# Performance work log

Measured on AMD Instinct MI355X. Metric: run time of the kernel, lower is better.

The kernel has to match this reference:

```python
import jax, jax.numpy as jnp
import numpy as np

N = 100000   # nodes per node type
E = 400000   # edges per relation
IN = 128     # input feature dim
HID = 128    # hidden_channels
H = 8        # heads
D = HID // H # head dim = 16
NEG_SLOPE = 0.2
BN_EPS = 1e-5


def setup_inputs() -> dict:
    key = jax.random.key(0)
    ks = jax.random.split(key, 24)
    f32 = jnp.float32
    def rn(k, shape, s):
        return jax.random.normal(k, shape, dtype=f32) * s
    inp = {
        'x_a': jax.random.normal(ks[0], (N, IN), dtype=f32),
        'x_b': jax.random.normal(ks[1], (N, IN), dtype=f32),
        'ei_ab': jax.random.randint(ks[2], (2, E), 0, N, dtype=jnp.int32),
        'ei_ba': jax.random.randint(ks[3], (2, E), 0, N, dtype=jnp.int32),
        'ei_aa': jax.random.randint(ks[4], (2, E), 0, N, dtype=jnp.int32),
        'ei_bb': jax.random.randint(ks[5], (2, E), 0, N, dtype=jnp.int32),
        # per-node-type projections (PyG Linear, with bias)
        'W_a': rn(ks[6], (IN, HID), 0.08), 'b_a': jnp.zeros((HID,), f32),
        'W_b': rn(ks[7], (IN, HID), 0.08), 'b_b': jnp.zeros((HID,), f32),
        # per-relation node-level attention vectors [H, D]
        'att_ab_s': rn(ks[8], (H, D), 0.2), 'att_ab_d': rn(ks[9], (H, D), 0.2),
        'att_ba_s': rn(ks[10], (H, D), 0.2), 'att_ba_d': rn(ks[11], (H, D), 0.2),
        'att_aa_s': rn(ks[12], (H, D), 0.2), 'att_aa_d': rn(ks[13], (H, D), 0.2),
        'att_bb_s': rn(ks[14], (H, D), 0.2), 'att_bb_d': rn(ks[15], (H, D), 0.2),
        # semantic-level attention: k_lin (Linear HID->HID) and query q
        'Wk': rn(ks[16], (HID, HID), 0.08), 'bk': jnp.zeros((HID,), f32),
        'q': rn(ks[17], (HID,), 0.2),
        # shared BatchNorm1d affine params
        'gamma': jnp.ones((HID,), f32), 'beta': jnp.zeros((HID,), f32),
    }
    return inp


def _edge_attn(h_src, h_dst, ei, att_s, att_d, n_dst):
    # GAT-style node-level attention for one relation (PyG HANConv message path)
    src, dst = ei[0], ei[1]
    a = (h_src * att_s).sum(-1)[src] + (h_dst * att_d).sum(-1)[dst]  # [E, H]
    a = jax.nn.leaky_relu(a, NEG_SLOPE)
    amax = jax.ops.segment_max(a, dst, num_segments=n_dst)            # [n_dst, H]
    amax = jnp.where(jnp.isfinite(amax), amax, 0.0)
    ex = jnp.exp(a - amax[dst])
    denom = jax.ops.segment_sum(ex, dst, num_segments=n_dst)[dst] + 1e-16
    w = ex / denom                                                    # segment softmax
    out = jax.ops.segment_sum(w[:, :, None] * h_src[src], dst, num_segments=n_dst)
    return jax.nn.relu(out.reshape(n_dst, H * D))                     # [n_dst, HID]


def _semantic(outs, Wk, bk, q):
    # semantic-level attention over relations targeting the same dst type
    st = jnp.stack(outs)                                   # [K, N, HID]
    score = (jnp.tanh(st @ Wk + bk).mean(axis=1) * q).sum(-1)  # [K]
    attn = jax.nn.softmax(score)
    return jnp.einsum('k,knf->nf', attn, st)


def _bn(x, gamma, beta):
    # BatchNorm1d in training mode: batch stats, biased variance
    mu = x.mean(axis=0)
    var = ((x - mu) ** 2).mean(axis=0)
    return (x - mu) * jax.lax.rsqrt(var + BN_EPS) * gamma + beta


def reference(x_a, x_b, ei_ab, ei_ba, ei_aa, ei_bb, W_a, b_a, W_b, b_b,
              att_ab_s, att_ab_d, att_ba_s, att_ba_d, att_aa_s, att_aa_d,
              att_bb_s, att_bb_d, Wk, bk, q, gamma, beta):
    h_a = (x_a @ W_a + b_a).reshape(N, H, D)
    h_b = (x_b @ W_b + b_b).reshape(N, H, D)
    o_ab = _edge_attn(h_a, h_b, ei_ab, att_ab_s, att_ab_d, N)  # dst b
    o_bb = _edge_attn(h_b, h_b, ei_bb, att_bb_s, att_bb_d, N)  # dst b
    o_ba = _edge_attn(h_b, h_a, ei_ba, att_ba_s, att_ba_d, N)  # dst a
    o_aa = _edge_attn(h_a, h_a, ei_aa, att_aa_s, att_aa_d, N)  # dst a
    out_a = _semantic([o_ba, o_aa], Wk, bk, q)
    out_b = _semantic([o_ab, o_bb], Wk, bk, q)
    return _bn(out_a, gamma, beta), _bn(out_b, gamma, beta)
```

## Files before the change

### kernel.cpp

```cpp
#include <hip/hip_runtime.h>

using u16 = unsigned short;
using u32 = unsigned int;
using bf16x8 = __attribute__((ext_vector_type(8))) short;
using f32x4  = __attribute__((ext_vector_type(4))) float;

__device__ __forceinline__ float bf2f(u16 v) { return __uint_as_float(((u32)v) << 16); }
__device__ __forceinline__ float blo(u32 u) { return __uint_as_float(u << 16); }
__device__ __forceinline__ float bhi(u32 u) { return __uint_as_float(u & 0xffff0000u); }
__device__ __forceinline__ u16 f2bf(float f) {
  u32 u = __float_as_uint(f);
  u += 0x7fffu + ((u >> 16) & 1u);
  return (u16)(u >> 16);
}
__device__ __forceinline__ float fast_tanh(float x) {
  float cx = fminf(fmaxf(x, -9.f), 9.f);
  float e = __expf(2.f * cx);
  return (e - 1.f) / (e + 1.f);
}

__global__ __launch_bounds__(256) void fused1_kernel(
    const float* __restrict__ x_a, const float* __restrict__ x_b,
    const float* __restrict__ W_a, const float* __restrict__ W_b,
    const float* __restrict__ b_a, const float* __restrict__ b_b,
    const float* __restrict__ at0a, const float* __restrict__ at1a,
    const float* __restrict__ at2a, const float* __restrict__ at3a,
    const float* __restrict__ at0b, const float* __restrict__ at1b,
    const float* __restrict__ at2b, const float* __restrict__ at3b,
    u16* __restrict__ ha, u16* __restrict__ hb,
    float* __restrict__ a0a, float* __restrict__ a1a,
    float* __restrict__ a2a, float* __restrict__ a3a,
    float* __restrict__ a0b, float* __restrict__ a1b,
    float* __restrict__ a2b, float* __restrict__ a3b,
    const int* __restrict__ e0, const int* __restrict__ e1,
    const int* __restrict__ e2, const int* __restrict__ e3,
    const float* __restrict__ Wk, u16* __restrict__ WkT,
    int* __restrict__ cnt,
    int N, int E, int gproj, int gE, int interleave)
{
  __shared__ __align__(16) u16 WTl[128 * 136];
  const int tid = threadIdx.x;
  const int bid = blockIdx.x;
  const int nP = 2 * gproj, nH = 4 * gE;

  int role, idx;
  if (bid >= nP + nH) { role = 2; idx = bid - nP - nH; }
  else if (interleave) {
    int slot = bid % 3, grp = bid / 3;
    if (slot == 0) { role = 0; idx = grp; }
    else           { role = 1; idx = grp * 2 + slot - 1; }
  } else {
    if (bid < nP) { role = 0; idx = bid; }
    else          { role = 1; idx = bid - nP; }
  }

  if (role == 1) {
    const int r = idx & 3, ex = idx >> 2;
    const int* ei = (r == 0) ? e0 : (r == 1) ? e1 : (r == 2) ? e2 : e3;
    int e = ex * 256 + tid;
    if (e < E) atomicAdd(&cnt[r * N + ei[E + e]], 1);
    return;
  }
  if (role == 2) {
    int i2 = idx * 256 + tid;
    int k = i2 >> 7, n = i2 & 127;
    WkT[n * 128 + k] = f2bf(Wk[i2]);
    return;
  }

  const int ty = idx >= gproj;
  const int bx = idx - (ty ? gproj : 0);
  const float* x    = ty ? x_b : x_a;
  const float* W    = ty ? W_b : W_a;
  const float* bias = ty ? b_b : b_a;
  const float* att0 = ty ? at0b : at0a;
  const float* att1 = ty ? at1b : at1a;
  const float* att2 = ty ? at2b : at2a;
  const float* att3 = ty ? at3b : at3a;
  u16* h_out = ty ? hb : ha;
  float* al0 = ty ? a0b : a0a;
  float* al1 = ty ? a1b : a1a;
  float* al2 = ty ? a2b : a2a;
  float* al3 = ty ? a3b : a3a;

  const float4* Wg = (const float4*)W;
#pragma unroll
  for (int i = 0; i < 16; ++i) {
    int id = tid + 256 * i;
    int k = id >> 5, n4 = (id & 31) << 2;
    float4 v = Wg[id];
    WTl[(n4 + 0) * 136 + k] = f2bf(v.x);
    WTl[(n4 + 1) * 136 + k] = f2bf(v.y);
    WTl[(n4 + 2) * 136 + k] = f2bf(v.z);
    WTl[(n4 + 3) * 136 + k] = f2bf(v.w);
  }
  __syncthreads();

  const int lane = tid & 63, wl = tid >> 6;
  const int col = lane & 15, g = lane >> 4;
  const int nb = bx * 64 + wl * 16;
  const int node = nb + col;
  const bool ok = node < N;

  const int arow = min(node, N - 1);
  const float* xr = x + (size_t)arow * 128;
  bf16x8 xh[4], xlo[4];
#pragma unroll
  for (int t = 0; t < 4; ++t) {
    float4 u = *(const float4*)&xr[t * 32 + g * 8];
    float4 v = *(const float4*)&xr[t * 32 + g * 8 + 4];
    float e[8] = {u.x, u.y, u.z, u.w, v.x, v.y, v.z, v.w};
    bf16x8 h8, l8;
#pragma unroll
    for (int j = 0; j < 8; ++j) {
      u16 hbt = f2bf(e[j]);
      h8[j] = (short)hbt;
      l8[j] = (short)f2bf(e[j] - bf2f(hbt));
    }
    xh[t] = h8; xlo[t] = l8;
  }

  f32x4 acc[8];
#pragma unroll
  for (int c = 0; c < 8; ++c) {
    float4 bv = *(const float4*)&bias[c * 16 + g * 4];
    acc[c] = (f32x4){bv.x, bv.y, bv.z, bv.w};
  }

#pragma unroll
  for (int c = 0; c < 8; ++c) {
    const u16* wrow = &WTl[(c * 16 + col) * 136];
#pragma unroll
    for (int t = 0; t < 4; ++t) {
      bf16x8 wf = *(const bf16x8*)&wrow[t * 32 + g * 8];
      acc[c] = __builtin_amdgcn_mfma_f32_16x16x32_bf16(wf, xh[t],  acc[c], 0, 0, 0);
      acc[c] = __builtin_amdgcn_mfma_f32_16x16x32_bf16(wf, xlo[t], acc[c], 0, 0, 0);
    }
  }

  if (ok) {
#pragma unroll
    for (int c = 0; c < 8; ++c) {
      uint2 hv;
      hv.x = (u32)f2bf(acc[c][0]) | ((u32)f2bf(acc[c][1]) << 16);
      hv.y = (u32)f2bf(acc[c][2]) | ((u32)f2bf(acc[c][3]) << 16);
      *(uint2*)(h_out + (size_t)node * 128 + c * 16 + g * 4) = hv;
    }
  }

#pragma unroll
  for (int c = 0; c < 8; ++c) {
    float4 a0v = *(const float4*)&att0[c * 16 + g * 4];
    float4 a1v = *(const float4*)&att1[c * 16 + g * 4];
    float4 a2v = *(const float4*)&att2[c * 16 + g * 4];
    float4 a3v = *(const float4*)&att3[c * 16 + g * 4];
    float p0 = acc[c][0] * a0v.x + acc[c][1] * a0v.y + acc[c][2] * a0v.z + acc[c][3] * a0v.w;
    float p1 = acc[c][0] * a1v.x + acc[c][1] * a1v.y + acc[c][2] * a1v.z + acc[c][3] * a1v.w;
    float p2 = acc[c][0] * a2v.x + acc[c][1] * a2v.y + acc[c][2] * a2v.z + acc[c][3] * a2v.w;
    float p3 = acc[c][0] * a3v.x + acc[c][1] * a3v.y + acc[c][2] * a3v.z + acc[c][3] * a3v.w;
    p0 += __shfl_xor(p0, 16); p0 += __shfl_xor(p0, 32);
    p1 += __shfl_xor(p1, 16); p1 += __shfl_xor(p1, 32);
    p2 += __shfl_xor(p2, 16); p2 += __shfl_xor(p2, 32);
    p3 += __shfl_xor(p3, 16); p3 += __shfl_xor(p3, 32);
    if (ok && g == 0) {
      al0[node * 8 + c] = p0;
      al1[node * 8 + c] = p1;
      al2[node * 8 + c] = p2;
      al3[node * 8 + c] = p3;
    }
  }
}

__global__ __launch_bounds__(256) void scan1_kernel(int* __restrict__ data, int M,
                                                    int* __restrict__ bsum)
{
  __shared__ int ls[256];
  const int tid = threadIdx.x;
  const int base = blockIdx.x * 2048 + tid * 8;
  int v[8]; int s = 0;
#pragma unroll
  for (int j = 0; j < 8; ++j) v[j] = (base + j < M) ? data[base + j] : 0;
#pragma unroll
  for (int j = 0; j < 8; ++j) { int t = v[j]; v[j] = s; s += t; }
  ls[tid] = s;
  __syncthreads();
  for (int off = 1; off < 256; off <<= 1) {
    int t = (tid >= off) ? ls[tid - off] : 0;
    __syncthreads();
    ls[tid] += t;
    __syncthreads();
  }
  int texcl = ls[tid] - s;
#pragma unroll
  for (int j = 0; j < 8; ++j)
    if (base + j < M) data[base + j] = v[j] + texcl;
  if (tid == 255) bsum[blockIdx.x] = ls[255];
}

__global__ __launch_bounds__(256) void scan2_kernel(int* __restrict__ bsum, int G1)
{
  __shared__ int ls[256];
  const int tid = threadIdx.x;
  int v = (tid < G1) ? bsum[tid] : 0;
  ls[tid] = v;
  __syncthreads();
  for (int off = 1; off < 256; off <<= 1) {
    int t = (tid >= off) ? ls[tid - off] : 0;
    __syncthreads();
    ls[tid] += t;
    __syncthreads();
  }
  if (tid < G1) bsum[tid] = ls[tid] - v;
}

__global__ __launch_bounds__(256) void scan3_kernel(int* __restrict__ data,
                                                    const int* __restrict__ bsum, int M,
                                                    int* __restrict__ cursor)
{
  const int add = bsum[blockIdx.x];
  const int base = blockIdx.x * 2048 + threadIdx.x * 8;
#pragma unroll
  for (int j = 0; j < 8; ++j) {
    int i = base + j;
    if (i < M) { int t = data[i] + add; data[i] = t; cursor[i] = t; }
  }
}

__global__ __launch_bounds__(256) void scatter_kernel(
    const int* __restrict__ e0, const int* __restrict__ e1,
    const int* __restrict__ e2, const int* __restrict__ e3,
    int E, int N, int* __restrict__ cursor, int* __restrict__ ssrc)
{
  const int r = blockIdx.y;
  const int* ei = (r == 0) ? e0 : (r == 1) ? e1 : (r == 2) ? e2 : e3;
  int e = blockIdx.x * 256 + threadIdx.x;
  if (e >= E) return;
  int s = ei[e], d = ei[E + e];
  int p = atomicAdd(&cursor[r * N + d], 1);
  ssrc[p] = s;
}

__global__ __launch_bounds__(256) void aggregate_kernel(
    const int* __restrict__ off, const int* __restrict__ ssrc,
    const float* __restrict__ aS0, const float* __restrict__ aS1,
    const float* __restrict__ aS2, const float* __restrict__ aS3,
    const float* __restrict__ aD0, const float* __restrict__ aD1,
    const float* __restrict__ aD2, const float* __restrict__ aD3,
    const u16* __restrict__ h0, const u16* __restrict__ h1,
    const u16* __restrict__ h2, const u16* __restrict__ h3,
    u32* __restrict__ o0, u32* __restrict__ o1,
    u32* __restrict__ o2, u32* __restrict__ o3,
    int N, int E)
{
  const int r = blockIdx.y;
  const float* aS = (r == 0) ? aS0 : (r == 1) ? aS1 : (r == 2) ? aS2 : aS3;
  const float* aD = (r == 0) ? aD0 : (r == 1) ? aD1 : (r == 2) ? aD2 : aD3;
  const u16*   h  = (r == 0) ? h0  : (r == 1) ? h1  : (r == 2) ? h2  : h3;
  u32*         o  = (r == 0) ? o0  : (r == 1) ? o1  : (r == 2) ? o2  : o3;

  const int wave = threadIdx.x >> 6, lane = threadIdx.x & 63;
  const int n = blockIdx.x * 4 + wave;
  if (n >= N) return;
  const int head = lane >> 3;
  const int idx = r * N + n;
  const int p0 = off[idx];
  const int p1 = (idx + 1 < 4 * N) ? off[idx + 1] : 4 * E;
  const float aDv = aD[n * 8 + head];
  const u32* h32 = (const u32*)h;

  float acc0 = 0.f, acc1 = 0.f, den = 0.f;
  int p = p0;
  for (; p + 4 <= p1; p += 4) {
    const int s0 = ssrc[p], s1 = ssrc[p + 1], s2 = ssrc[p + 2], s3 = ssrc[p + 3];
    const float g0 = aS[s0 * 8 + head];
    const float g1 = aS[s1 * 8 + head];
    const float g2 = aS[s2 * 8 + head];
    const float g3 = aS[s3 * 8 + head];
    const u32 v0 = h32[s0 * 64 + lane];
    const u32 v1 = h32[s1 * 64 + lane];
    const u32 v2 = h32[s2 * 64 + lane];
    const u32 v3 = h32[s3 * 64 + lane];
    float l0 = g0 + aDv, l1 = g1 + aDv, l2 = g2 + aDv, l3 = g3 + aDv;
    l0 = fmaxf(l0, 0.2f * l0); l1 = fmaxf(l1, 0.2f * l1);
    l2 = fmaxf(l2, 0.2f * l2); l3 = fmaxf(l3, 0.2f * l3);
    const float w0 = __expf(l0), w1 = __expf(l1);
    const float w2 = __expf(l2), w3 = __expf(l3);
    den += (w0 + w1) + (w2 + w3);
    acc0 += w0 * blo(v0) + w1 * blo(v1) + w2 * blo(v2) + w3 * blo(v3);
    acc1 += w0 * bhi(v0) + w1 * bhi(v1) + w2 * bhi(v2) + w3 * bhi(v3);
  }
  const int rem = p1 - p;
  if (rem > 0) {
    const int s0 = ssrc[p];
    const int s1 = ssrc[(rem > 1) ? p + 1 : p];
    const int s2 = ssrc[(rem > 2) ? p + 2 : p];
    const float g0 = aS[s0 * 8 + head];
    const float g1 = aS[s1 * 8 + head];
    const float g2 = aS[s2 * 8 + head];
    const u32 v0 = h32[s0 * 64 + lane];
    const u32 v1 = h32[s1 * 64 + lane];
    const u32 v2 = h32[s2 * 64 + lane];
    float l0 = g0 + aDv, l1 = g1 + aDv, l2 = g2 + aDv;
    l0 = fmaxf(l0, 0.2f * l0); l1 = fmaxf(l1, 0.2f * l1); l2 = fmaxf(l2, 0.2f * l2);
    const float w0 = __expf(l0);
    const float w1 = (rem > 1) ? __expf(l1) : 0.f;
    const float w2 = (rem > 2) ? __expf(l2) : 0.f;
    den += w0 + w1 + w2;
    acc0 += w0 * blo(v0) + w1 * blo(v1) + w2 * blo(v2);
    acc1 += w0 * bhi(v0) + w1 * bhi(v1) + w2 * bhi(v2);
  }
  const float inv = 1.f / (den + 1e-16f);
  const float r0 = fmaxf(acc0 * inv, 0.f);
  const float r1 = fmaxf(acc1 * inv, 0.f);
  o[n * 64 + lane] = (u32)f2bf(r0) | ((u32)f2bf(r1) << 16);
}

__global__ __launch_bounds__(256) void fused2_kernel(
    const u32* __restrict__ oba, const u32* __restrict__ oaa,
    const u32* __restrict__ oab, const u32* __restrict__ obb,
    const u16* __restrict__ WkT, const float* __restrict__ bk,
    const float* __restrict__ q, float* __restrict__ scores,
    float* __restrict__ sums_a, float* __restrict__ sums_b,
    int N, int R, int gproj)
{
  __shared__ __align__(16) u16 WTl[128 * 136];
  __shared__ float red[4];
  const int tid = threadIdx.x;
  const int bid = blockIdx.x;

  if (bid < 512) {
    const int t = bid >> 8, bx = bid & 255;
    const u32* p0 = t ? oab : oba;
    const u32* p1 = t ? obb : oaa;
    float* sums = t ? sums_b : sums_a;
    const int tc = tid & 31, tr = tid >> 5;
    float s0[4] = {0,0,0,0}, s1[4] = {0,0,0,0};
    float q00[4] = {0,0,0,0}, q11[4] = {0,0,0,0}, q01[4] = {0,0,0,0};
    const int rend = min((bx + 1) * R, N);
    for (int row = bx * R + tr; row < rend; row += 8) {
      uint2 v0 = *(const uint2*)&p0[row * 64 + tc * 2];
      uint2 v1 = *(const uint2*)&p1[row * 64 + tc * 2];
      float r0[4] = {blo(v0.x), bhi(v0.x), blo(v0.y), bhi(v0.y)};
      float r1[4] = {blo(v1.x), bhi(v1.x), blo(v1.y), bhi(v1.y)};
#pragma unroll
      for (int j = 0; j < 4; ++j) {
        s0[j] += r0[j]; s1[j] += r1[j];
        q00[j] += r0[j] * r0[j]; q11[j] += r1[j] * r1[j];
        q01[j] += r0[j] * r1[j];
      }
    }
    float* sm = (float*)WTl;
    for (int i = tid; i < 640; i += 256) sm[i] = 0.f;
    __syncthreads();
#pragma unroll
    for (int j = 0; j < 4; ++j) {
      int f = tc * 4 + j;
      atomicAdd(&sm[f], s0[j]);
      atomicAdd(&sm[128 + f], s1[j]);
      atomicAdd(&sm[256 + f], q00[j]);
      atomicAdd(&sm[384 + f], q11[j]);
      atomicAdd(&sm[512 + f], q01[j]);
    }
    __syncthreads();
    for (int i = tid; i < 640; i += 256) atomicAdd(&sums[i], sm[i]);
    return;
  }

  const int sid = bid - 512;
  const int rel = sid & 3, bx = sid >> 2;
  const u32* op = (rel == 0) ? oba : (rel == 1) ? oaa : (rel == 2) ? oab : obb;
  const u16* o = (const u16*)op;

  const uint4* Wg = (const uint4*)WkT;
#pragma unroll
  for (int i = 0; i < 8; ++i) {
    int id = tid + 256 * i;
    uint4 v = Wg[id];
    int n = id >> 4, k8 = (id & 15) << 3;
    *(uint4*)&WTl[n * 136 + k8] = v;
  }
  __syncthreads();

  const int lane = tid & 63, wl = tid >> 6;
  const int col = lane & 15, g = lane >> 4;
  const int nb = bx * 64 + wl * 16;

  float bv[8], qv[8];
#pragma unroll
  for (int c = 0; c < 8; ++c) {
    bv[c] = bk[c * 16 + col];
    qv[c] = q[c * 16 + col];
  }

  const int arow = min(nb + col, N - 1);
  const u16* orow = o + (size_t)arow * 128;
  bf16x8 af[4];
#pragma unroll
  for (int t = 0; t < 4; ++t) af[t] = *(const bf16x8*)&orow[t * 32 + g * 8];

  f32x4 acc[8];
#pragma unroll
  for (int c = 0; c < 8; ++c) acc[c] = (f32x4){bv[c], bv[c], bv[c], bv[c]};

#pragma unroll
  for (int c = 0; c < 8; ++c) {
    const u16* wrow = &WTl[(c * 16 + col) * 136];
#pragma unroll
    for (int t = 0; t < 4; ++t) {
      bf16x8 bf = *(const bf16x8*)&wrow[t * 32 + g * 8];
      acc[c] = __builtin_amdgcn_mfma_f32_16x16x32_bf16(af[t], bf, acc[c], 0, 0, 0);
    }
  }

  float p = 0.f;
  const int rowbase = nb + g * 4;
#pragma unroll
  for (int c = 0; c < 8; ++c) {
#pragma unroll
    for (int i = 0; i < 4; ++i) {
      int node = rowbase + i;
      if (node < N) p += fast_tanh(acc[c][i]) * qv[c];
    }
  }
#pragma unroll
  for (int off = 32; off > 0; off >>= 1) p += __shfl_down(p, off);
  if (lane == 0) red[wl] = p;
  __syncthreads();
  if (tid == 0) atomicAdd(&scores[rel], red[0] + red[1] + red[2] + red[3]);
}

__global__ __launch_bounds__(256) void bn_final_kernel(
    const u32* __restrict__ oba, const u32* __restrict__ oaa,
    const u32* __restrict__ oab, const u32* __restrict__ obb,
    const float* __restrict__ scores, const float* __restrict__ sums_a,
    const float* __restrict__ sums_b,
    const float* __restrict__ gamma, const float* __restrict__ beta,
    float* __restrict__ out, int N)
{
  const int t = blockIdx.y;
  const u32* o0 = t ? oab : oba;
  const u32* o1 = t ? obb : oaa;
  const float* sums = t ? sums_b : sums_a;
  float* op = out + (size_t)t * N * 128;

  const float invN = 1.f / (float)N;
  const float sc0 = scores[2 * t] * invN, sc1 = scores[2 * t + 1] * invN;
  const float m = fmaxf(sc0, sc1);
  const float e0 = expf(sc0 - m), e1 = expf(sc1 - m);
  const float einv = 1.f / (e0 + e1);
  const float a0 = e0 * einv, a1 = e1 * einv;

  __shared__ float scale[128], shift[128];
  if (threadIdx.x < 128) {
    int f = threadIdx.x;
    float S0 = sums[f], S1 = sums[128 + f];
    float Q00 = sums[256 + f], Q11 = sums[384 + f], Q01 = sums[512 + f];
    float mu = (a0 * S0 + a1 * S1) * invN;
    float msq = (a0 * a0 * Q00 + 2.f * a0 * a1 * Q01 + a1 * a1 * Q11) * invN;
    float var = fmaxf(msq - mu * mu, 0.f);
    float rs = rsqrtf(var + 1e-5f);
    float gm = gamma[f] * rs;
    scale[f] = gm;
    shift[f] = beta[f] - mu * gm;
  }
  __syncthreads();
  size_t total = (size_t)N * 128;
  for (size_t base = ((size_t)blockIdx.x * 256 + threadIdx.x) * 8; base < total;
       base += (size_t)gridDim.x * 2048) {
    int f0 = (int)(base & 127);
    uint4 p = *(const uint4*)&o0[base >> 1];
    uint4 q = *(const uint4*)&o1[base >> 1];
    float4 r0, r1;
    r0.x = (a0 * blo(p.x) + a1 * blo(q.x)) * scale[f0 + 0] + shift[f0 + 0];
    r0.y = (a0 * bhi(p.x) + a1 * bhi(q.x)) * scale[f0 + 1] + shift[f0 + 1];
    r0.z = (a0 * blo(p.y) + a1 * blo(q.y)) * scale[f0 + 2] + shift[f0 + 2];
    r0.w = (a0 * bhi(p.y) + a1 * bhi(q.y)) * scale[f0 + 3] + shift[f0 + 3];
    r1.x = (a0 * blo(p.z) + a1 * blo(q.z)) * scale[f0 + 4] + shift[f0 + 4];
    r1.y = (a0 * bhi(p.z) + a1 * bhi(q.z)) * scale[f0 + 5] + shift[f0 + 5];
    r1.z = (a0 * blo(p.w) + a1 * blo(q.w)) * scale[f0 + 6] + shift[f0 + 6];
    r1.w = (a0 * bhi(p.w) + a1 * bhi(q.w)) * scale[f0 + 7] + shift[f0 + 7];
    *(float4*)&op[base] = r0;
    *(float4*)&op[base + 4] = r1;
  }
}

extern "C" void kernel_launch(void* const* d_in, const int* in_sizes, int n_in,
                              void* d_out, int out_size, void* d_ws, size_t ws_size,
                              hipStream_t stream)
{
  const float* x_a      = (const float*)d_in[0];
  const float* x_b      = (const float*)d_in[1];
  const int* ei_ab      = (const int*)d_in[2];
  const int* ei_ba      = (const int*)d_in[3];
  const int* ei_aa      = (const int*)d_in[4];
  const int* ei_bb      = (const int*)d_in[5];
  const float* W_a      = (const float*)d_in[6];
  const float* b_a      = (const float*)d_in[7];
  const float* W_b      = (const float*)d_in[8];
  const float* b_b      = (const float*)d_in[9];
  const float* att_ab_s = (const float*)d_in[10];
  const float* att_ab_d = (const float*)d_in[11];
  const float* att_ba_s = (const float*)d_in[12];
  const float* att_ba_d = (const float*)d_in[13];
  const float* att_aa_s = (const float*)d_in[14];
  const float* att_aa_d = (const float*)d_in[15];
  const float* att_bb_s = (const float*)d_in[16];
  const float* att_bb_d = (const float*)d_in[17];
  const float* Wk       = (const float*)d_in[18];
  const float* bk       = (const float*)d_in[19];
  const float* q        = (const float*)d_in[20];
  const float* gamma    = (const float*)d_in[21];
  const float* beta     = (const float*)d_in[22];

  const int N = in_sizes[0] / 128;
  const int E = in_sizes[2] / 2;

  char* wp = (char*)d_ws;
  auto alloc = [&](size_t bytes) -> void* {
    void* p = (void*)wp;
    wp += (bytes + 255) & ~(size_t)255;
    return p;
  };
  u16* h_a = (u16*)alloc((size_t)N * 128 * 2);
  u16* h_b = (u16*)alloc((size_t)N * 128 * 2);
  float* A[8];
  for (int i = 0; i < 8; ++i) A[i] = (float*)alloc((size_t)N * 8 * 4);
  int* off    = (int*)alloc((size_t)4 * N * 4);
  int* cursor = (int*)alloc((size_t)4 * N * 4);
  int* bsum   = (int*)alloc(1024);
  int* ssrc   = (int*)alloc((size_t)4 * E * 4);
  u32* o_ab = (u32*)alloc((size_t)N * 64 * 4);
  u32* o_ba = (u32*)alloc((size_t)N * 64 * 4);
  u32* o_aa = (u32*)alloc((size_t)N * 64 * 4);
  u32* o_bb = (u32*)alloc((size_t)N * 64 * 4);
  float* scores = (float*)alloc(16);
  float* sums_a = (float*)alloc(2560);
  float* sums_b = (float*)alloc(2560);
  u16* WT_k = (u16*)alloc(128 * 128 * 2);
  if ((size_t)(wp - (char*)d_ws) > ws_size) return;

  hipMemsetAsync(off, 0, (size_t)4 * N * 4, stream);
  hipMemsetAsync(scores, 0, 5376, stream);

  const int gproj = (N + 63) / 64;
  const int gE = (E + 255) / 256;
  const int interleave = (gE == gproj) ? 1 : 0;
  const int g1total = 2 * gproj + 4 * gE + 64;
  fused1_kernel<<<g1total, 256, 0, stream>>>(
      x_a, x_b, W_a, W_b, b_a, b_b,
      att_ab_s, att_aa_s, att_aa_d, att_ba_d,
      att_ab_d, att_bb_s, att_bb_d, att_ba_s,
      h_a, h_b,
      A[0], A[1], A[2], A[3], A[4], A[5], A[6], A[7],
      ei_ab, ei_ba, ei_aa, ei_bb,
      Wk, WT_k, off, N, E, gproj, gE, interleave);

  const int M = 4 * N;
  const int G1 = (M + 2047) / 2048;
  scan1_kernel<<<G1, 256, 0, stream>>>(off, M, bsum);
  scan2_kernel<<<1, 256, 0, stream>>>(bsum, G1);
  scan3_kernel<<<G1, 256, 0, stream>>>(off, bsum, M, cursor);
  dim3 gsc(gE, 4);
  scatter_kernel<<<gsc, 256, 0, stream>>>(ei_ab, ei_ba, ei_aa, ei_bb, E, N, cursor, ssrc);

  dim3 gag((N + 3) / 4, 4);
  aggregate_kernel<<<gag, 256, 0, stream>>>(
      off, ssrc,
      A[0], A[7], A[1], A[5],
      A[4], A[3], A[2], A[6],
      h_a, h_b, h_a, h_b,
      o_ab, o_ba, o_aa, o_bb, N, E);

  const int R = (N + 255) / 256;
  const int g2total = 512 + 4 * gproj;
  fused2_kernel<<<g2total, 256, 0, stream>>>(
      o_ba, o_aa, o_ab, o_bb, WT_k, bk, q, scores, sums_a, sums_b, N, R, gproj);

  float* out = (float*)d_out;
  dim3 gbf(1024, 2);
  bn_final_kernel<<<gbf, 256, 0, stream>>>(o_ba, o_aa, o_ab, o_bb, scores,
                                           sums_a, sums_b, gamma, beta, out, N);
}
```

Baseline: 654.3 us.

## Pretranspose weights in a prep kernel, read from global, fold scan2 into scan3

Adds a small kernel that converts W_a, W_b and Wk to transposed bf16 once. The projection and semantic GEMM blocks then read weight fragments straight from global memory (L2-resident) instead of each block staging the full weight into LDS with a __syncthreads. This removes per-block conversion work and frees LDS, which may raise occupancy. The separate scan2 launch is dropped: each scan3 block reduces the preceding block sums itself. The tradeoffs are one extra launch for the prep kernel and uncoalesced global weight reads inside the MFMA loop.

```diff
diff --git a/kernel.cpp b/kernel.cpp
--- a/kernel.cpp
+++ b/kernel.cpp
@@ -19,9 +19,22 @@
   return (e - 1.f) / (e + 1.f);
 }
 
+__global__ __launch_bounds__(256) void wprep_kernel(
+    const float* __restrict__ Wa, const float* __restrict__ Wb,
+    const float* __restrict__ Wk,
+    u16* __restrict__ Ta, u16* __restrict__ Tb, u16* __restrict__ Tk)
+{
+  const int w = blockIdx.y;
+  const float* W = (w == 0) ? Wa : (w == 1) ? Wb : Wk;
+  u16* T = (w == 0) ? Ta : (w == 1) ? Tb : Tk;
+  int idx = blockIdx.x * 256 + threadIdx.x;
+  int k = idx >> 7, n = idx & 127;
+  T[n * 128 + k] = f2bf(W[idx]);
+}
+
 __global__ __launch_bounds__(256) void fused1_kernel(
     const float* __restrict__ x_a, const float* __restrict__ x_b,
-    const float* __restrict__ W_a, const float* __restrict__ W_b,
+    const u16* __restrict__ WTa, const u16* __restrict__ WTb,
     const float* __restrict__ b_a, const float* __restrict__ b_b,
     const float* __restrict__ at0a, const float* __restrict__ at1a,
     const float* __restrict__ at2a, const float* __restrict__ at3a,
@@ -34,18 +47,15 @@
     float* __restrict__ a2b, float* __restrict__ a3b,
     const int* __restrict__ e0, const int* __restrict__ e1,
     const int* __restrict__ e2, const int* __restrict__ e3,
-    const float* __restrict__ Wk, u16* __restrict__ WkT,
     int* __restrict__ cnt,
     int N, int E, int gproj, int gE, int interleave)
 {
-  __shared__ __align__(16) u16 WTl[128 * 136];
   const int tid = threadIdx.x;
   const int bid = blockIdx.x;
-  const int nP = 2 * gproj, nH = 4 * gE;
+  const int nP = 2 * gproj;
 
   int role, idx;
-  if (bid >= nP + nH) { role = 2; idx = bid - nP - nH; }
-  else if (interleave) {
+  if (interleave) {
     int slot = bid % 3, grp = bid / 3;
     if (slot == 0) { role = 0; idx = grp; }
     else           { role = 1; idx = grp * 2 + slot - 1; }
@@ -61,17 +71,11 @@
     if (e < E) atomicAdd(&cnt[r * N + ei[E + e]], 1);
     return;
   }
-  if (role == 2) {
-    int i2 = idx * 256 + tid;
-    int k = i2 >> 7, n = i2 & 127;
-    WkT[n * 128 + k] = f2bf(Wk[i2]);
-    return;
-  }
 
   const int ty = idx >= gproj;
   const int bx = idx - (ty ? gproj : 0);
   const float* x    = ty ? x_b : x_a;
-  const float* W    = ty ? W_b : W_a;
+  const u16*  WT    = ty ? WTb : WTa;
   const float* bias = ty ? b_b : b_a;
   const float* att0 = ty ? at0b : at0a;
   const float* att1 = ty ? at1b : at1a;
@@ -83,19 +87,6 @@
   float* al2 = ty ? a2b : a2a;
   float* al3 = ty ? a3b : a3a;
 
-  const float4* Wg = (const float4*)W;
-#pragma unroll
-  for (int i = 0; i < 16; ++i) {
-    int id = tid + 256 * i;
-    int k = id >> 5, n4 = (id & 31) << 2;
-    float4 v = Wg[id];
-    WTl[(n4 + 0) * 136 + k] = f2bf(v.x);
-    WTl[(n4 + 1) * 136 + k] = f2bf(v.y);
-    WTl[(n4 + 2) * 136 + k] = f2bf(v.z);
-    WTl[(n4 + 3) * 136 + k] = f2bf(v.w);
-  }
-  __syncthreads();
-
   const int lane = tid & 63, wl = tid >> 6;
   const int col = lane & 15, g = lane >> 4;
   const int nb = bx * 64 + wl * 16;
@@ -129,7 +120,7 @@
 
 #pragma unroll
   for (int c = 0; c < 8; ++c) {
-    const u16* wrow = &WTl[(c * 16 + col) * 136];
+    const u16* wrow = WT + (c * 16 + col) * 128;
 #pragma unroll
     for (int t = 0; t < 4; ++t) {
       bf16x8 wf = *(const bf16x8*)&wrow[t * 32 + g * 8];
@@ -197,28 +188,19 @@
   if (tid == 255) bsum[blockIdx.x] = ls[255];
 }
 
-__global__ __launch_bounds__(256) void scan2_kernel(int* __restrict__ bsum, int G1)
-{
-  __shared__ int ls[256];
-  const int tid = threadIdx.x;
-  int v = (tid < G1) ? bsum[tid] : 0;
-  ls[tid] = v;
-  __syncthreads();
-  for (int off = 1; off < 256; off <<= 1) {
-    int t = (tid >= off) ? ls[tid - off] : 0;
-    __syncthreads();
-    ls[tid] += t;
-    __syncthreads();
-  }
-  if (tid < G1) bsum[tid] = ls[tid] - v;
-}
-
 __global__ __launch_bounds__(256) void scan3_kernel(int* __restrict__ data,
                                                     const int* __restrict__ bsum, int M,
                                                     int* __restrict__ cursor)
 {
-  const int add = bsum[blockIdx.x];
-  const int base = blockIdx.x * 2048 + threadIdx.x * 8;
+  __shared__ int rs[4];
+  const int tid = threadIdx.x;
+  int v = (tid < (int)blockIdx.x) ? bsum[tid] : 0;
+#pragma unroll
+  for (int off = 32; off > 0; off >>= 1) v += __shfl_down(v, off);
+  if ((tid & 63) == 0) rs[tid >> 6] = v;
+  __syncthreads();
+  const int add = rs[0] + rs[1] + rs[2] + rs[3];
+  const int base = blockIdx.x * 2048 + tid * 8;
 #pragma unroll
   for (int j = 0; j < 8; ++j) {
     int i = base + j;
@@ -323,7 +305,7 @@
     float* __restrict__ sums_a, float* __restrict__ sums_b,
     int N, int R, int gproj)
 {
-  __shared__ __align__(16) u16 WTl[128 * 136];
+  __shared__ float sm[640];
   __shared__ float red[4];
   const int tid = threadIdx.x;
   const int bid = blockIdx.x;
@@ -349,7 +331,6 @@
         q01[j] += r0[j] * r1[j];
       }
     }
-    float* sm = (float*)WTl;
     for (int i = tid; i < 640; i += 256) sm[i] = 0.f;
     __syncthreads();
 #pragma unroll
@@ -371,16 +352,6 @@
   const u32* op = (rel == 0) ? oba : (rel == 1) ? oaa : (rel == 2) ? oab : obb;
   const u16* o = (const u16*)op;
 
-  const uint4* Wg = (const uint4*)WkT;
-#pragma unroll
-  for (int i = 0; i < 8; ++i) {
-    int id = tid + 256 * i;
-    uint4 v = Wg[id];
-    int n = id >> 4, k8 = (id & 15) << 3;
-    *(uint4*)&WTl[n * 136 + k8] = v;
-  }
-  __syncthreads();
-
   const int lane = tid & 63, wl = tid >> 6;
   const int col = lane & 15, g = lane >> 4;
   const int nb = bx * 64 + wl * 16;
@@ -404,7 +375,7 @@
 
 #pragma unroll
   for (int c = 0; c < 8; ++c) {
-    const u16* wrow = &WTl[(c * 16 + col) * 136];
+    const u16* wrow = WkT + (c * 16 + col) * 128;
 #pragma unroll
     for (int t = 0; t < 4; ++t) {
       bf16x8 bf = *(const bf16x8*)&wrow[t * 32 + g * 8];
@@ -536,29 +507,33 @@
   float* scores = (float*)alloc(16);
   float* sums_a = (float*)alloc(2560);
   float* sums_b = (float*)alloc(2560);
+  u16* WT_a = (u16*)alloc(128 * 128 * 2);
+  u16* WT_b = (u16*)alloc(128 * 128 * 2);
   u16* WT_k = (u16*)alloc(128 * 128 * 2);
   if ((size_t)(wp - (char*)d_ws) > ws_size) return;
 
   hipMemsetAsync(off, 0, (size_t)4 * N * 4, stream);
   hipMemsetAsync(scores, 0, 5376, stream);
+
+  dim3 gw(64, 3);
+  wprep_kernel<<<gw, 256, 0, stream>>>(W_a, W_b, Wk, WT_a, WT_b, WT_k);
 
   const int gproj = (N + 63) / 64;
   const int gE = (E + 255) / 256;
   const int interleave = (gE == gproj) ? 1 : 0;
-  const int g1total = 2 * gproj + 4 * gE + 64;
+  const int g1total = 2 * gproj + 4 * gE;
   fused1_kernel<<<g1total, 256, 0, stream>>>(
-      x_a, x_b, W_a, W_b, b_a, b_b,
+      x_a, x_b, WT_a, WT_b, b_a, b_b,
       att_ab_s, att_aa_s, att_aa_d, att_ba_d,
       att_ab_d, att_bb_s, att_bb_d, att_ba_s,
       h_a, h_b,
       A[0], A[1], A[2], A[3], A[4], A[5], A[6], A[7],
       ei_ab, ei_ba, ei_aa, ei_bb,
-      Wk, WT_k, off, N, E, gproj, gE, interleave);
+      off, N, E, gproj, gE, interleave);
 
   const int M = 4 * N;
   const int G1 = (M + 2047) / 2048;
   scan1_kernel<<<G1, 256, 0, stream>>>(off, M, bsum);
-  scan2_kernel<<<1, 256, 0, stream>>>(bsum, G1);
   scan3_kernel<<<G1, 256, 0, stream>>>(off, bsum, M, cursor);
   dim3 gsc(gE, 4);
   scatter_kernel<<<gsc, 256, 0, stream>>>(ei_ab, ei_ba, ei_aa, ei_bb, E, N, cursor, ssrc);
```

Result: slower. 703.8 us (+7.6%).
